# Kernel tuning notes

Measured on AMD Instinct MI355X. Metric: run time of the kernel, lower is better.

## Reference

```python
import jax, jax.numpy as jnp
import numpy as np

B, S, D, H, F, R = 4, 128, 512, 8, 2048, 8
DH = D // H
THRESH = 0.1  # hardcoded in the torch module


def _ln(x, g, b):
    m = x.mean(-1, keepdims=True)
    v = ((x - m) ** 2).mean(-1, keepdims=True)
    return (x - m) * jax.lax.rsqrt(v + 1e-5) * g + b


def setup_inputs() -> dict:
    key = jax.random.key(0)
    ks = jax.random.split(key, 12)
    w = lambda k, shape, std: jax.random.normal(k, shape, jnp.float32) * std
    s = 1.0 / np.sqrt(D)
    qk_std = 2.0 / np.sqrt(D)  # peaky attention so adjacency threshold fires
    return {
        "x": jax.random.normal(ks[0], (B, S, D), jnp.float32),
        "ln1_g": jnp.ones(D, jnp.float32), "ln1_b": jnp.zeros(D, jnp.float32),
        "wq": w(ks[1], (D, D), qk_std), "bq": jnp.zeros(D, jnp.float32),
        "wk": w(ks[2], (D, D), qk_std), "bk": jnp.zeros(D, jnp.float32),
        "wv": w(ks[3], (D, D), s), "bv": jnp.zeros(D, jnp.float32),
        "wo": w(ks[4], (D, D), s), "bo": jnp.zeros(D, jnp.float32),
        "w1": w(ks[5], (D, F), s), "b1": jnp.zeros(F, jnp.float32),
        "w2": w(ks[6], (F, D), 1.0 / np.sqrt(F)), "b2": jnp.zeros(D, jnp.float32),
        "rc_w1": w(ks[7], (2 * D, D), 1.0 / np.sqrt(2 * D)), "rc_b1": jnp.zeros(D, jnp.float32),
        "rc_w2": w(ks[8], (D, R), s), "rc_b2": jnp.zeros(R, jnp.float32),
        "kg_w": w(ks[9], (R, D, D), s),
        "s2n_w": w(ks[10], (D, D), s), "s2n_b": jnp.zeros(D, jnp.float32),
        "ln2_g": jnp.ones(D, jnp.float32), "ln2_b": jnp.zeros(D, jnp.float32),
    }


def reference(x, ln1_g, ln1_b, wq, bq, wk, bk, wv, bv, wo, bo,
              w1, b1, w2, b2, rc_w1, rc_b1, rc_w2, rc_b2,
              kg_w, s2n_w, s2n_b, ln2_g, ln2_b):
    # pre-norm attention
    xn = _ln(x, ln1_g, ln1_b)
    q = (xn @ wq + bq).reshape(B, S, H, DH)
    k = (xn @ wk + bk).reshape(B, S, H, DH)
    v = (xn @ wv + bv).reshape(B, S, H, DH)
    scores = jnp.einsum('bihd,bjhd->bhij', q, k) / np.sqrt(DH)
    attn = jax.nn.softmax(scores, axis=-1)                  # [B,H,S,S]
    ctx = jnp.einsum('bhij,bjhd->bihd', attn, v).reshape(B, S, D)
    attn_out = ctx @ wo + bo
    # FFN -> neural_understanding (no residual, as in source)
    nu = jax.nn.relu(attn_out @ w1 + b1) @ w2 + b2          # [B,S,D]
    # dynamic edge extraction, expressed as a dense mask (jit-safe)
    am = attn.mean(axis=1)                                  # [B,S,S]
    adj = (am > THRESH) & (~jnp.eye(S, dtype=bool))         # u != v
    # relation classifier on every (u,v) pair; mask selects real edges
    a_part = nu @ rc_w1[:D]                                 # concept1 half
    b_part = nu @ rc_w1[D:]                                 # concept2 half
    h = jax.nn.relu(a_part[:, :, None, :] + b_part[:, None, :, :] + rc_b1)  # [B,S,S,D]
    logits = h @ rc_w2 + rc_b2                              # [B,S,S,R]
    pred = jnp.argmax(logits, axis=-1)
    valid = adj & (pred != 0)                               # relation 0 == NONE
    oh = jax.nn.one_hot(pred, R, dtype=nu.dtype) * valid[..., None].astype(nu.dtype)
    # RGCN-style knowledge graph conv: message u -> v with per-relation weight
    transformed = jnp.einsum('bud,rde->bure', nu, kg_w)     # [B,S,R,D]
    agg = jnp.einsum('buvr,bure->bve', oh, transformed)     # [B,S,D]
    reasoned = nu + agg
    neural_result = reasoned @ s2n_w + s2n_b
    out = _ln(x + neural_result, ln2_g, ln2_b)
    return out
```

## Files before the change

kernel.cpp:

```cpp
#include <hip/hip_runtime.h>
#include <hip/hip_bf16.h>

#define B_ 4
#define S_ 128
#define D_ 512
#define H_ 8
#define DH_ 64
#define F_ 2048
#define R_ 8
#define BS_ (B_ * S_)
#define BSD_ (BS_ * D_)
#define E_ 262144

typedef __attribute__((ext_vector_type(8))) short short8;
typedef __attribute__((ext_vector_type(4))) float f32x4;
typedef __attribute__((ext_vector_type(4))) unsigned short ushort4v;

__device__ __forceinline__ void split2(float a, unsigned short& h, unsigned short& l) {
    unsigned u = __float_as_uint(a);
    unsigned hr = (u + 0x7FFFu + ((u >> 16) & 1u)) >> 16;
    h = (unsigned short)hr;
    float lo = a - __uint_as_float(hr << 16);
    unsigned u2 = __float_as_uint(lo);
    l = (unsigned short)((u2 + 0x7FFFu + ((u2 >> 16) & 1u)) >> 16);
}

struct TDesc { const float* s; unsigned short* h; unsigned short* l; int K; int N; int off; };
struct TPack { TDesc d[10]; };

__global__ void prep_kernel(TPack p, int nt, const float* __restrict__ x,
                            const float* __restrict__ g, const float* __restrict__ be,
                            unsigned short* __restrict__ xh, unsigned short* __restrict__ xl) {
    __shared__ float tr[32][33];
    __shared__ float red[256];
    int bid = blockIdx.x;
    if (bid < nt) {
        int wi = 0;
#pragma unroll
        for (int i = 1; i < 10; ++i) if (bid >= p.d[i].off) wi = i;
        const TDesc dd = p.d[wi];
        int t = bid - dd.off;
        int ntk = dd.K / 32;
        int tk = t % ntk, tn = t / ntk;
        int k0 = tk * 32, n0 = tn * 32;
        int col = threadIdx.x & 31, rg = threadIdx.x >> 5;
#pragma unroll
        for (int i = 0; i < 4; ++i) {
            int row = rg * 4 + i;
            tr[row][col] = dd.s[(size_t)(k0 + row) * dd.N + n0 + col];
        }
        __syncthreads();
#pragma unroll
        for (int i = 0; i < 4; ++i) {
            int n = n0 + rg * 4 + i;
            int k = k0 + col;
            unsigned short h, l;
            split2(tr[col][rg * 4 + i], h, l);
            dd.h[(size_t)n * dd.K + k] = h;
            dd.l[(size_t)n * dd.K + k] = l;
        }
    } else {
        int row = bid - nt;
        int t = threadIdx.x;
        const float* xr = x + (size_t)row * D_;
        float v0 = xr[t], v1 = xr[t + 256];
        red[t] = v0 + v1;
        __syncthreads();
        for (int off = 128; off > 0; off >>= 1) { if (t < off) red[t] += red[t + off]; __syncthreads(); }
        float mean = red[0] * (1.0f / D_);
        __syncthreads();
        float d0 = v0 - mean, d1 = v1 - mean;
        red[t] = d0 * d0 + d1 * d1;
        __syncthreads();
        for (int off = 128; off > 0; off >>= 1) { if (t < off) red[t] += red[t + off]; __syncthreads(); }
        float rs = rsqrtf(red[0] * (1.0f / D_) + 1e-5f);
        float o0 = d0 * rs * g[t] + be[t];
        float o1 = d1 * rs * g[t + 256] + be[t + 256];
        unsigned short h, l;
        split2(o0, h, l); xh[(size_t)row * D_ + t] = h;       xl[(size_t)row * D_ + t] = l;
        split2(o1, h, l); xh[(size_t)row * D_ + t + 256] = h; xl[(size_t)row * D_ + t + 256] = l;
    }
}

struct GemmLds {
    unsigned short A[2][2][64][32];
    unsigned short B[2][2][64][32];
};

__device__ __forceinline__ void gload16(const unsigned short* g, unsigned short* l) {
    __builtin_amdgcn_global_load_lds(
        (const __attribute__((address_space(1))) void*)g,
        (__attribute__((address_space(3))) void*)l, 16, 0, 0);
}

__device__ __forceinline__ void mgemm_core(const unsigned short* __restrict__ Ath,
                                           const unsigned short* __restrict__ Atl,
                                           const unsigned short* __restrict__ Bth,
                                           const unsigned short* __restrict__ Btl,
                                           int K, int rowBase, int colBase,
                                           int kStart, int nsteps,
                                           f32x4 acc[2][2], GemmLds* L) {
    int tid = threadIdx.x;
    int w = tid >> 6, lane = tid & 63;
    int lm = lane & 15, quad = lane >> 4;
    int wm = (w & 1) * 32, wn = (w >> 1) * 32;
    int rS = tid >> 2, kcS = (tid & 3) * 8;
    int wb = w * 512;
    size_t aoff = (size_t)(rowBase + rS) * K + kStart + kcS;
    size_t boff = (size_t)(colBase + rS) * K + kStart + kcS;
    gload16(&Ath[aoff], &L->A[0][0][0][0] + wb);
    gload16(&Atl[aoff], &L->A[0][1][0][0] + wb);
    gload16(&Bth[boff], &L->B[0][0][0][0] + wb);
    gload16(&Btl[boff], &L->B[0][1][0][0] + wb);
    __syncthreads();
    for (int s = 0; s < nsteps; ++s) {
        int p = s & 1;
        if (s + 1 < nsteps) {
            int pn = p ^ 1;
            size_t ao = aoff + (size_t)(s + 1) * 32;
            size_t bo = boff + (size_t)(s + 1) * 32;
            gload16(&Ath[ao], &L->A[pn][0][0][0] + wb);
            gload16(&Atl[ao], &L->A[pn][1][0][0] + wb);
            gload16(&Bth[bo], &L->B[pn][0][0][0] + wb);
            gload16(&Btl[bo], &L->B[pn][1][0][0] + wb);
        }
        short8 ah[2], al[2], bh[2], bl[2];
#pragma unroll
        for (int t = 0; t < 2; ++t) {
            ah[t] = *(const short8*)&L->A[p][0][wm + t * 16 + lm][quad * 8];
            al[t] = *(const short8*)&L->A[p][1][wm + t * 16 + lm][quad * 8];
            bh[t] = *(const short8*)&L->B[p][0][wn + t * 16 + lm][quad * 8];
            bl[t] = *(const short8*)&L->B[p][1][wn + t * 16 + lm][quad * 8];
        }
#pragma unroll
        for (int tm = 0; tm < 2; ++tm)
#pragma unroll
            for (int tn = 0; tn < 2; ++tn) {
                acc[tm][tn] = __builtin_amdgcn_mfma_f32_16x16x32_bf16(ah[tm], bh[tn], acc[tm][tn], 0, 0, 0);
                acc[tm][tn] = __builtin_amdgcn_mfma_f32_16x16x32_bf16(ah[tm], bl[tn], acc[tm][tn], 0, 0, 0);
                acc[tm][tn] = __builtin_amdgcn_mfma_f32_16x16x32_bf16(al[tm], bh[tn], acc[tm][tn], 0, 0, 0);
            }
        __syncthreads();
    }
}

__global__ __launch_bounds__(256) void mgemm_kernel(const unsigned short* __restrict__ Ath,
                                                    const unsigned short* __restrict__ Atl,
                                                    const unsigned short* __restrict__ Bth,
                                                    const unsigned short* __restrict__ Btl,
                                                    const float* __restrict__ bias,
                                                    float* __restrict__ Cf,
                                                    unsigned short* __restrict__ Ch,
                                                    unsigned short* __restrict__ Cl,
                                                    int N, int K, int relu) {
    __shared__ GemmLds L;
    int tid = threadIdx.x;
    int w = tid >> 6, lane = tid & 63;
    int lm = lane & 15, quad = lane >> 4;
    int wm = (w & 1) * 32, wn = (w >> 1) * 32;
    int rowBase = blockIdx.y * 64, colBase = blockIdx.x * 64;
    f32x4 acc[2][2] = {};
    mgemm_core(Ath, Atl, Bth, Btl, K, rowBase, colBase, 0, K / 32, acc, &L);
#pragma unroll
    for (int tm = 0; tm < 2; ++tm)
#pragma unroll
        for (int tn = 0; tn < 2; ++tn) {
            int col = colBase + wn + tn * 16 + lm;
            float bi = bias ? bias[col] : 0.f;
#pragma unroll
            for (int r = 0; r < 4; ++r) {
                int row = rowBase + wm + tm * 16 + quad * 4 + r;
                float v = acc[tm][tn][r] + bi;
                if (relu) v = fmaxf(v, 0.f);
                size_t o = (size_t)row * N + col;
                if (Cf) Cf[o] = v;
                if (Ch) {
                    unsigned short sh, sl;
                    split2(v, sh, sl);
                    Ch[o] = sh; Cl[o] = sl;
                }
            }
        }
}

__global__ __launch_bounds__(256) void mgemm_zw_kernel(const unsigned short* __restrict__ Ath,
                                                       const unsigned short* __restrict__ Atl,
                                                       const unsigned short* __restrict__ Bth,
                                                       const unsigned short* __restrict__ Btl,
                                                       const float* __restrict__ b0,
                                                       const float* __restrict__ b1,
                                                       const float* __restrict__ b2,
                                                       float* __restrict__ Cbase,
                                                       int M, int N, int K) {
    __shared__ GemmLds L;
    int z = blockIdx.z;
    const unsigned short* bth = Bth + (size_t)z * K * N;
    const unsigned short* btl = Btl + (size_t)z * K * N;
    const float* bias = (z == 0) ? b0 : (z == 1) ? b1 : b2;
    float* C = Cbase + (size_t)z * M * N;
    int tid = threadIdx.x;
    int w = tid >> 6, lane = tid & 63;
    int lm = lane & 15, quad = lane >> 4;
    int wm = (w & 1) * 32, wn = (w >> 1) * 32;
    int rowBase = blockIdx.y * 64, colBase = blockIdx.x * 64;
    f32x4 acc[2][2] = {};
    mgemm_core(Ath, Atl, bth, btl, K, rowBase, colBase, 0, K / 32, acc, &L);
#pragma unroll
    for (int tm = 0; tm < 2; ++tm)
#pragma unroll
        for (int tn = 0; tn < 2; ++tn) {
            int col = colBase + wn + tn * 16 + lm;
            float bi = bias ? bias[col] : 0.f;
#pragma unroll
            for (int r = 0; r < 4; ++r) {
                int row = rowBase + wm + tm * 16 + quad * 4 + r;
                C[(size_t)row * N + col] = acc[tm][tn][r] + bi;
            }
        }
}

__global__ __launch_bounds__(256) void mgemm_part_kernel(const unsigned short* __restrict__ Ath,
                                                         const unsigned short* __restrict__ Atl,
                                                         const unsigned short* __restrict__ Bth,
                                                         const unsigned short* __restrict__ Btl,
                                                         float* __restrict__ Cbase,
                                                         int M, int N, int K) {
    __shared__ GemmLds L;
    int ks = gridDim.z, z = blockIdx.z;
    int kLen = K / ks, kStart = z * kLen;
    float* C = Cbase + (size_t)z * M * N;
    int tid = threadIdx.x;
    int w = tid >> 6, lane = tid & 63;
    int lm = lane & 15, quad = lane >> 4;
    int wm = (w & 1) * 32, wn = (w >> 1) * 32;
    int rowBase = blockIdx.y * 64, colBase = blockIdx.x * 64;
    f32x4 acc[2][2] = {};
    mgemm_core(Ath, Atl, Bth, Btl, K, rowBase, colBase, kStart, kLen / 32, acc, &L);
#pragma unroll
    for (int tm = 0; tm < 2; ++tm)
#pragma unroll
        for (int tn = 0; tn < 2; ++tn) {
            int col = colBase + wn + tn * 16 + lm;
#pragma unroll
            for (int r = 0; r < 4; ++r) {
                int row = rowBase + wm + tm * 16 + quad * 4 + r;
                C[(size_t)row * N + col] = acc[tm][tn][r];
            }
        }
}

__global__ void reduce4_kernel(const float* __restrict__ part, const float* __restrict__ b2,
                               float* __restrict__ nu,
                               unsigned short* __restrict__ nh, unsigned short* __restrict__ nl) {
    int base = blockIdx.x * 1024 + threadIdx.x * 4;
    f32x4 s = *(const f32x4*)&b2[base & (D_ - 1)];
#pragma unroll
    for (int z = 0; z < 4; ++z) s += *(const f32x4*)&part[(size_t)z * BSD_ + base];
    *(f32x4*)&nu[base] = s;
    ushort4v hv, lv;
#pragma unroll
    for (int i = 0; i < 4; ++i) { unsigned short h, l; split2(s[i], h, l); hv[i] = h; lv[i] = l; }
    *(ushort4v*)&nh[base] = hv;
    *(ushort4v*)&nl[base] = lv;
}

__global__ void reduce8_kernel(const float* __restrict__ part, const float* __restrict__ nu,
                               unsigned short* __restrict__ rh, unsigned short* __restrict__ rl) {
    int base = blockIdx.x * 1024 + threadIdx.x * 4;
    f32x4 s = *(const f32x4*)&nu[base];
#pragma unroll
    for (int z = 0; z < 8; ++z) s += *(const f32x4*)&part[(size_t)z * BSD_ + base];
    ushort4v hv, lv;
#pragma unroll
    for (int i = 0; i < 4; ++i) { unsigned short h, l; split2(s[i], h, l); hv[i] = h; lv[i] = l; }
    *(ushort4v*)&rh[base] = hv;
    *(ushort4v*)&rl[base] = lv;
}

__global__ __launch_bounds__(512) void attn_fused_kernel(const float* __restrict__ q,
                                                         const float* __restrict__ k,
                                                         const float* __restrict__ v,
                                                         unsigned short* __restrict__ ch,
                                                         unsigned short* __restrict__ cl,
                                                         int* __restrict__ ecount,
                                                         int* __restrict__ elist) {
    __shared__ float qsm[H_][DH_];
    __shared__ float psm[H_][S_];
    int h = threadIdx.x >> 6, lane = threadIdx.x & 63;
    int blk = blockIdx.x;
    int i = blk & (S_ - 1);
    int b = blk >> 7;
    const float* qrow = q + (size_t)(b * S_ + i) * D_ + h * DH_;
    qsm[h][lane] = qrow[lane];
    __syncthreads();
    float s0 = 0.f, s1 = 0.f;
    const float* k0p = k + (size_t)(b * S_ + lane) * D_ + h * DH_;
    const float* k1p = k0p + (size_t)64 * D_;
#pragma unroll 8
    for (int d = 0; d < DH_; ++d) {
        float qd = qsm[h][d];
        s0 += qd * k0p[d];
        s1 += qd * k1p[d];
    }
    s0 *= 0.125f; s1 *= 0.125f;
    float m = fmaxf(s0, s1);
#pragma unroll
    for (int off = 32; off > 0; off >>= 1) m = fmaxf(m, __shfl_xor(m, off));
    float e0 = __expf(s0 - m), e1 = __expf(s1 - m);
    float sum = e0 + e1;
#pragma unroll
    for (int off = 32; off > 0; off >>= 1) sum += __shfl_xor(sum, off);
    float inv = 1.f / sum;
    psm[h][lane] = e0 * inv;
    psm[h][lane + 64] = e1 * inv;
    __syncthreads();
    if (threadIdx.x < S_) {
        int j = threadIdx.x;
        float s = 0.f;
#pragma unroll
        for (int hh = 0; hh < H_; ++hh) s += psm[hh][j];
        s *= (1.0f / H_);
        if (s > 0.1f && i != j) {
            int p = atomicAdd(ecount, 1);
            elist[p] = blk * S_ + j;
        }
    }
    const float* vbase = v + (size_t)b * S_ * D_ + h * DH_ + lane;
    float acc = 0.f;
    for (int j = 0; j < S_; ++j) acc += psm[h][j] * vbase[(size_t)j * D_];
    unsigned short sh, sl;
    split2(acc, sh, sl);
    size_t o = (size_t)(b * S_ + i) * D_ + h * DH_ + lane;
    ch[o] = sh; cl[o] = sl;
}

__global__ __launch_bounds__(256) void edge_kernel(const float* __restrict__ a_part,
                                                   const float* __restrict__ b_part,
                                                   const float* __restrict__ rc_b1,
                                                   const float* __restrict__ rc_w2,
                                                   const float* __restrict__ rc_b2,
                                                   const int* __restrict__ elist,
                                                   const int* __restrict__ ecount,
                                                   int* __restrict__ rel) {
    int w = threadIdx.x >> 6, lane = threadIdx.x & 63;
    int n = *ecount;
    for (int e = blockIdx.x * 4 + w; e < n; e += gridDim.x * 4) {
        int idx = elist[e];
        int vv = idx & (S_ - 1);
        int bu = idx >> 7;
        int u = bu & (S_ - 1);
        int b = bu >> 7;
        const float* ap = a_part + (size_t)(b * S_ + u) * D_;
        const float* bp = b_part + (size_t)(b * S_ + vv) * D_;
        float lp[R_];
#pragma unroll
        for (int r = 0; r < R_; ++r) lp[r] = 0.f;
#pragma unroll
        for (int jj = 0; jj < D_ / 64; ++jj) {
            int d = lane + jj * 64;
            float hv = fmaxf(ap[d] + bp[d] + rc_b1[d], 0.f);
#pragma unroll
            for (int r = 0; r < R_; ++r) lp[r] += hv * rc_w2[d * R_ + r];
        }
#pragma unroll
        for (int r = 0; r < R_; ++r) {
#pragma unroll
            for (int off = 32; off > 0; off >>= 1) lp[r] += __shfl_down(lp[r], off);
        }
        if (lane == 0) {
            float best = lp[0] + rc_b2[0];
            int bi = 0;
#pragma unroll
            for (int r = 1; r < R_; ++r) {
                float L = lp[r] + rc_b2[r];
                if (L > best) { best = L; bi = r; }
            }
            rel[idx] = bi;
        }
    }
}

__global__ __launch_bounds__(128) void mbuild_kernel(const float* __restrict__ nu,
                                                     const int* __restrict__ rel,
                                                     unsigned short* __restrict__ Mh,
                                                     unsigned short* __restrict__ Ml) {
    __shared__ float acc[R_ * D_];
    __shared__ int rl[S_];
    int blk = blockIdx.x;
    int vv = blk & (S_ - 1);
    int b = blk >> 7;
    int t = threadIdx.x;
    for (int i = t; i < R_ * D_; i += 128) acc[i] = 0.f;
    rl[t] = rel[((size_t)b * S_ + t) * S_ + vv];
    __syncthreads();
    for (int u = 0; u < S_; ++u) {
        int r = rl[u];
        if (r > 0) {
            const float* nurow = nu + (size_t)(b * S_ + u) * D_;
            float* arow = acc + r * D_;
#pragma unroll
            for (int jj = 0; jj < D_ / 128; ++jj) arow[t + jj * 128] += nurow[t + jj * 128];
        }
    }
    __syncthreads();
    unsigned short* Hrow = Mh + (size_t)blk * (R_ * D_);
    unsigned short* Lrow = Ml + (size_t)blk * (R_ * D_);
    for (int i = t; i < R_ * D_; i += 128) {
        unsigned short sh, sl;
        split2(acc[i], sh, sl);
        Hrow[i] = sh; Lrow[i] = sl;
    }
}

__global__ void ln2_kernel(const float* __restrict__ x, const float* __restrict__ y,
                           const float* __restrict__ g, const float* __restrict__ be,
                           float* __restrict__ out) {
    int row = blockIdx.x;
    int t = threadIdx.x;
    __shared__ float red[256];
    float v0 = x[row * D_ + t]       + y[row * D_ + t];
    float v1 = x[row * D_ + t + 256] + y[row * D_ + t + 256];
    red[t] = v0 + v1;
    __syncthreads();
    for (int off = 128; off > 0; off >>= 1) {
        if (t < off) red[t] += red[t + off];
        __syncthreads();
    }
    float mean = red[0] * (1.0f / D_);
    __syncthreads();
    float d0 = v0 - mean, d1 = v1 - mean;
    red[t] = d0 * d0 + d1 * d1;
    __syncthreads();
    for (int off = 128; off > 0; off >>= 1) {
        if (t < off) red[t] += red[t + off];
        __syncthreads();
    }
    float rs = rsqrtf(red[0] * (1.0f / D_) + 1e-5f);
    out[row * D_ + t]       = d0 * rs * g[t]       + be[t];
    out[row * D_ + t + 256] = d1 * rs * g[t + 256] + be[t + 256];
}

extern "C" void kernel_launch(void* const* d_in, const int* in_sizes, int n_in,
                              void* d_out, int out_size, void* d_ws, size_t ws_size,
                              hipStream_t stream) {
    const float* x     = (const float*)d_in[0];
    const float* ln1_g = (const float*)d_in[1];
    const float* ln1_b = (const float*)d_in[2];
    const float* wq    = (const float*)d_in[3];
    const float* bq    = (const float*)d_in[4];
    const float* wk    = (const float*)d_in[5];
    const float* bk    = (const float*)d_in[6];
    const float* wv    = (const float*)d_in[7];
    const float* bv    = (const float*)d_in[8];
    const float* wo    = (const float*)d_in[9];
    const float* bo    = (const float*)d_in[10];
    const float* w1    = (const float*)d_in[11];
    const float* b1    = (const float*)d_in[12];
    const float* w2    = (const float*)d_in[13];
    const float* b2    = (const float*)d_in[14];
    const float* rc_w1 = (const float*)d_in[15];
    const float* rc_b1 = (const float*)d_in[16];
    const float* rc_w2 = (const float*)d_in[17];
    const float* rc_b2 = (const float*)d_in[18];
    const float* kg_w  = (const float*)d_in[19];
    const float* s2n_w = (const float*)d_in[20];
    const float* s2n_b = (const float*)d_in[21];
    const float* ln2_g = (const float*)d_in[22];
    const float* ln2_b = (const float*)d_in[23];
    float* out = (float*)d_out;

    const int BS  = BS_;
    const int BSD = BSD_;

    unsigned short* wt = (unsigned short*)d_ws;
    unsigned short* qkv_h = wt;
    unsigned short* qkv_l = wt + 3 * E_;
    unsigned short* wo_h  = wt + 6 * E_;
    unsigned short* wo_l  = wt + 7 * E_;
    unsigned short* w1_h  = wt + 8 * E_;
    unsigned short* w1_l  = wt + 12 * E_;
    unsigned short* w2_h  = wt + 16 * E_;
    unsigned short* w2_l  = wt + 20 * E_;
    unsigned short* rc_h  = wt + 24 * E_;
    unsigned short* rc_l  = wt + 26 * E_;
    unsigned short* kg_h  = wt + 28 * E_;
    unsigned short* kg_l  = wt + 36 * E_;
    unsigned short* s2_h  = wt + 44 * E_;
    unsigned short* s2_l  = wt + 45 * E_;

    unsigned short* xn_h  = wt + 46 * E_;
    unsigned short* xn_l  = xn_h + BSD;
    unsigned short* ctx_h = xn_l + BSD;
    unsigned short* ctx_l = ctx_h + BSD;
    unsigned short* ao_h  = ctx_l + BSD;
    unsigned short* ao_l  = ao_h + BSD;
    unsigned short* hid_h = ao_l + BSD;
    unsigned short* hid_l = hid_h + (size_t)BS * F_;
    unsigned short* nu_h  = hid_l + (size_t)BS * F_;
    unsigned short* nu_l  = nu_h + BSD;
    unsigned short* mb_h  = nu_l + BSD;
    unsigned short* mb_l  = mb_h + (size_t)BS * R_ * D_;
    unsigned short* rs_h  = mb_l + (size_t)BS * R_ * D_;
    unsigned short* rs_l  = rs_h + BSD;

    float* fbase  = (float*)(rs_l + BSD);
    float* q      = fbase;
    float* v_     = q + 2 * BSD;
    float* apart  = q + 3 * BSD;
    float* nu     = apart + 2 * BSD;
    float* y      = nu + BSD;
    float* part4  = y + BSD;
    float* part8  = part4 + 4 * BSD;

    int* rel    = (int*)(part8 + 8 * BSD);
    int* ecount = rel + B_ * S_ * S_;
    int* elist  = ecount + 64;

    hipMemsetAsync(rel, 0, (size_t)(B_ * S_ * S_ + 64) * 4, stream);
    TPack tp;
    int off = 0;
    auto setd = [&](int i, const float* s, unsigned short* h, unsigned short* l, int K, int N) {
        tp.d[i] = TDesc{s, h, l, K, N, off};
        off += (K / 32) * (N / 32);
    };
    setd(0, wq, qkv_h,          qkv_l,          D_, D_);
    setd(1, wk, qkv_h + E_,     qkv_l + E_,     D_, D_);
    setd(2, wv, qkv_h + 2 * E_, qkv_l + 2 * E_, D_, D_);
    setd(3, wo, wo_h, wo_l, D_, D_);
    setd(4, w1, w1_h, w1_l, D_, F_);
    setd(5, w2, w2_h, w2_l, F_, D_);
    setd(6, rc_w1,            rc_h,      rc_l,      D_, D_);
    setd(7, rc_w1 + D_ * D_,  rc_h + E_, rc_l + E_, D_, D_);
    setd(8, kg_w, kg_h, kg_l, R_ * D_, D_);
    setd(9, s2n_w, s2_h, s2_l, D_, D_);
    hipLaunchKernelGGL(prep_kernel, dim3(off + BS), dim3(256), 0, stream, tp, off,
                       x, ln1_g, ln1_b, xn_h, xn_l);

    hipLaunchKernelGGL(mgemm_zw_kernel, dim3(D_ / 64, BS / 64, 3), dim3(256), 0, stream,
                       xn_h, xn_l, qkv_h, qkv_l, bq, bk, bv, q, BS, D_, D_);
    hipLaunchKernelGGL(attn_fused_kernel, dim3(BS), dim3(512), 0, stream,
                       q, q + BSD, v_, ctx_h, ctx_l, ecount, elist);
    hipLaunchKernelGGL(mgemm_kernel, dim3(D_ / 64, BS / 64), dim3(256), 0, stream,
                       ctx_h, ctx_l, wo_h, wo_l, bo, (float*)nullptr, ao_h, ao_l, D_, D_, 0);
    hipLaunchKernelGGL(mgemm_kernel, dim3(F_ / 64, BS / 64), dim3(256), 0, stream,
                       ao_h, ao_l, w1_h, w1_l, b1, (float*)nullptr, hid_h, hid_l, F_, D_, 1);
    hipLaunchKernelGGL(mgemm_part_kernel, dim3(D_ / 64, BS / 64, 4), dim3(256), 0, stream,
                       hid_h, hid_l, w2_h, w2_l, part4, BS, D_, F_);
    hipLaunchKernelGGL(reduce4_kernel, dim3(BSD / 1024), dim3(256), 0, stream,
                       part4, b2, nu, nu_h, nu_l);
    hipLaunchKernelGGL(mgemm_zw_kernel, dim3(D_ / 64, BS / 64, 2), dim3(256), 0, stream,
                       nu_h, nu_l, rc_h, rc_l, (const float*)nullptr, (const float*)nullptr,
                       (const float*)nullptr, apart, BS, D_, D_);
    hipLaunchKernelGGL(edge_kernel, dim3(256), dim3(256), 0, stream,
                       apart, apart + BSD, rc_b1, rc_w2, rc_b2, elist, ecount, rel);
    hipLaunchKernelGGL(mbuild_kernel, dim3(BS), dim3(128), 0, stream, nu, rel, mb_h, mb_l);
    hipLaunchKernelGGL(mgemm_part_kernel, dim3(D_ / 64, BS / 64, 8), dim3(256), 0, stream,
                       mb_h, mb_l, kg_h, kg_l, part8, BS, D_, R_ * D_);
    hipLaunchKernelGGL(reduce8_kernel, dim3(BSD / 1024), dim3(256), 0, stream,
                       part8, nu, rs_h, rs_l);
    hipLaunchKernelGGL(mgemm_kernel, dim3(D_ / 64, BS / 64), dim3(256), 0, stream,
                       rs_h, rs_l, s2_h, s2_l, s2n_b, y, (unsigned short*)nullptr,
                       (unsigned short*)nullptr, D_, D_, 0);
    hipLaunchKernelGGL(ln2_kernel, dim3(BS), dim3(256), 0, stream, x, y, ln2_g, ln2_b, out);
}
```

Measured before the change: 251.3 us.

## Unify GEMMs into split-K kernel with last-block atomic reduction

Replaces the separate GEMM, partial-GEMM and reduce kernels with one split-K kernel. Blocks write fp32 partials, and the last block for each tile, found through an atomic counter, sums them and applies bias, residual, relu and the bf16 split. This removes the two standalone reduce launches and raises block counts for the small 512x512 GEMMs to fill more CUs. The cost is extra partial-buffer traffic, thread fences, and a serialized reduction done by the last-arriving block.

```diff
diff --git a/kernel.cpp b/kernel.cpp
--- a/kernel.cpp
+++ b/kernel.cpp
@@ -144,23 +144,83 @@
     }
 }
 
-__global__ __launch_bounds__(256) void mgemm_kernel(const unsigned short* __restrict__ Ath,
-                                                    const unsigned short* __restrict__ Atl,
-                                                    const unsigned short* __restrict__ Bth,
-                                                    const unsigned short* __restrict__ Btl,
-                                                    const float* __restrict__ bias,
-                                                    float* __restrict__ Cf,
-                                                    unsigned short* __restrict__ Ch,
-                                                    unsigned short* __restrict__ Cl,
-                                                    int N, int K, int relu) {
+__global__ __launch_bounds__(256) void mg_kernel(const unsigned short* __restrict__ Ath,
+                                                 const unsigned short* __restrict__ Atl,
+                                                 const unsigned short* __restrict__ Bth,
+                                                 const unsigned short* __restrict__ Btl,
+                                                 const float* __restrict__ b0,
+                                                 const float* __restrict__ b1,
+                                                 const float* __restrict__ b2,
+                                                 const float* __restrict__ res,
+                                                 float* __restrict__ Cf,
+                                                 unsigned short* __restrict__ Ch,
+                                                 unsigned short* __restrict__ Cl,
+                                                 float* __restrict__ part,
+                                                 int* __restrict__ flags,
+                                                 int nz, int N, int K, int relu) {
     __shared__ GemmLds L;
+    __shared__ int smLast;
+    int ks = gridDim.z / nz;
+    int slab = blockIdx.z / ks, split = blockIdx.z - slab * ks;
+    int M = gridDim.y * 64;
+    const unsigned short* bth = Bth + (size_t)slab * K * N;
+    const unsigned short* btl = Btl + (size_t)slab * K * N;
+    const float* bias = (slab == 0) ? b0 : (slab == 1) ? b1 : b2;
+    size_t slabOff = (size_t)slab * M * N;
+    int kLen = K / ks;
     int tid = threadIdx.x;
     int w = tid >> 6, lane = tid & 63;
     int lm = lane & 15, quad = lane >> 4;
     int wm = (w & 1) * 32, wn = (w >> 1) * 32;
     int rowBase = blockIdx.y * 64, colBase = blockIdx.x * 64;
     f32x4 acc[2][2] = {};
-    mgemm_core(Ath, Atl, Bth, Btl, K, rowBase, colBase, 0, K / 32, acc, &L);
+    mgemm_core(Ath, Atl, bth, btl, K, rowBase, colBase, split * kLen, kLen / 32, acc, &L);
+
+    if (ks == 1) {
+#pragma unroll
+        for (int tm = 0; tm < 2; ++tm)
+#pragma unroll
+            for (int tn = 0; tn < 2; ++tn) {
+                int col = colBase + wn + tn * 16 + lm;
+                float bi = bias ? bias[col] : 0.f;
+#pragma unroll
+                for (int r = 0; r < 4; ++r) {
+                    int row = rowBase + wm + tm * 16 + quad * 4 + r;
+                    size_t o = (size_t)row * N + col;
+                    float v = acc[tm][tn][r] + bi;
+                    if (res) v += res[slabOff + o];
+                    if (relu) v = fmaxf(v, 0.f);
+                    if (Cf) Cf[slabOff + o] = v;
+                    if (Ch) {
+                        unsigned short sh, sl;
+                        split2(v, sh, sl);
+                        Ch[slabOff + o] = sh; Cl[slabOff + o] = sl;
+                    }
+                }
+            }
+        return;
+    }
+    float* myPart = part + (size_t)(slab * ks + split) * M * N;
+#pragma unroll
+    for (int tm = 0; tm < 2; ++tm)
+#pragma unroll
+        for (int tn = 0; tn < 2; ++tn) {
+            int col = colBase + wn + tn * 16 + lm;
+#pragma unroll
+            for (int r = 0; r < 4; ++r) {
+                int row = rowBase + wm + tm * 16 + quad * 4 + r;
+                myPart[(size_t)row * N + col] = acc[tm][tn][r];
+            }
+        }
+    __threadfence();
+    __syncthreads();
+    if (tid == 0) {
+        int fi = slab * gridDim.x * gridDim.y + blockIdx.y * gridDim.x + blockIdx.x;
+        smLast = (atomicAdd(&flags[fi], 1) == ks - 1);
+    }
+    __syncthreads();
+    if (!smLast) return;
+    __threadfence();
 #pragma unroll
     for (int tm = 0; tm < 2; ++tm)
 #pragma unroll
@@ -170,111 +230,19 @@
 #pragma unroll
             for (int r = 0; r < 4; ++r) {
                 int row = rowBase + wm + tm * 16 + quad * 4 + r;
-                float v = acc[tm][tn][r] + bi;
-                if (relu) v = fmaxf(v, 0.f);
                 size_t o = (size_t)row * N + col;
-                if (Cf) Cf[o] = v;
+                float s = res ? res[slabOff + o] : bi;
+                for (int z = 0; z < ks; ++z)
+                    s += part[(size_t)(slab * ks + z) * M * N + o];
+                if (relu) s = fmaxf(s, 0.f);
+                if (Cf) Cf[slabOff + o] = s;
                 if (Ch) {
                     unsigned short sh, sl;
-                    split2(v, sh, sl);
-                    Ch[o] = sh; Cl[o] = sl;
+                    split2(s, sh, sl);
+                    Ch[slabOff + o] = sh; Cl[slabOff + o] = sl;
                 }
             }
         }
-}
-
-__global__ __launch_bounds__(256) void mgemm_zw_kernel(const unsigned short* __restrict__ Ath,
-                                                       const unsigned short* __restrict__ Atl,
-                                                       const unsigned short* __restrict__ Bth,
-                                                       const unsigned short* __restrict__ Btl,
-                                                       const float* __restrict__ b0,
-                                                       const float* __restrict__ b1,
-                                                       const float* __restrict__ b2,
-                                                       float* __restrict__ Cbase,
-                                                       int M, int N, int K) {
-    __shared__ GemmLds L;
-    int z = blockIdx.z;
-    const unsigned short* bth = Bth + (size_t)z * K * N;
-    const unsigned short* btl = Btl + (size_t)z * K * N;
-    const float* bias = (z == 0) ? b0 : (z == 1) ? b1 : b2;
-    float* C = Cbase + (size_t)z * M * N;
-    int tid = threadIdx.x;
-    int w = tid >> 6, lane = tid & 63;
-    int lm = lane & 15, quad = lane >> 4;
-    int wm = (w & 1) * 32, wn = (w >> 1) * 32;
-    int rowBase = blockIdx.y * 64, colBase = blockIdx.x * 64;
-    f32x4 acc[2][2] = {};
-    mgemm_core(Ath, Atl, bth, btl, K, rowBase, colBase, 0, K / 32, acc, &L);
-#pragma unroll
-    for (int tm = 0; tm < 2; ++tm)
-#pragma unroll
-        for (int tn = 0; tn < 2; ++tn) {
-            int col = colBase + wn + tn * 16 + lm;
-            float bi = bias ? bias[col] : 0.f;
-#pragma unroll
-            for (int r = 0; r < 4; ++r) {
-                int row = rowBase + wm + tm * 16 + quad * 4 + r;
-                C[(size_t)row * N + col] = acc[tm][tn][r] + bi;
-            }
-        }
-}
-
-__global__ __launch_bounds__(256) void mgemm_part_kernel(const unsigned short* __restrict__ Ath,
-                                                         const unsigned short* __restrict__ Atl,
-                                                         const unsigned short* __restrict__ Bth,
-                                                         const unsigned short* __restrict__ Btl,
-                                                         float* __restrict__ Cbase,
-                                                         int M, int N, int K) {
-    __shared__ GemmLds L;
-    int ks = gridDim.z, z = blockIdx.z;
-    int kLen = K / ks, kStart = z * kLen;
-    float* C = Cbase + (size_t)z * M * N;
-    int tid = threadIdx.x;
-    int w = tid >> 6, lane = tid & 63;
-    int lm = lane & 15, quad = lane >> 4;
-    int wm = (w & 1) * 32, wn = (w >> 1) * 32;
-    int rowBase = blockIdx.y * 64, colBase = blockIdx.x * 64;
-    f32x4 acc[2][2] = {};
-    mgemm_core(Ath, Atl, Bth, Btl, K, rowBase, colBase, kStart, kLen / 32, acc, &L);
-#pragma unroll
-    for (int tm = 0; tm < 2; ++tm)
-#pragma unroll
-        for (int tn = 0; tn < 2; ++tn) {
-            int col = colBase + wn + tn * 16 + lm;
-#pragma unroll
-            for (int r = 0; r < 4; ++r) {
-                int row = rowBase + wm + tm * 16 + quad * 4 + r;
-                C[(size_t)row * N + col] = acc[tm][tn][r];
-            }
-        }
-}
-
-__global__ void reduce4_kernel(const float* __restrict__ part, const float* __restrict__ b2,
-                               float* __restrict__ nu,
-                               unsigned short* __restrict__ nh, unsigned short* __restrict__ nl) {
-    int base = blockIdx.x * 1024 + threadIdx.x * 4;
-    f32x4 s = *(const f32x4*)&b2[base & (D_ - 1)];
-#pragma unroll
-    for (int z = 0; z < 4; ++z) s += *(const f32x4*)&part[(size_t)z * BSD_ + base];
-    *(f32x4*)&nu[base] = s;
-    ushort4v hv, lv;
-#pragma unroll
-    for (int i = 0; i < 4; ++i) { unsigned short h, l; split2(s[i], h, l); hv[i] = h; lv[i] = l; }
-    *(ushort4v*)&nh[base] = hv;
-    *(ushort4v*)&nl[base] = lv;
-}
-
-__global__ void reduce8_kernel(const float* __restrict__ part, const float* __restrict__ nu,
-                               unsigned short* __restrict__ rh, unsigned short* __restrict__ rl) {
-    int base = blockIdx.x * 1024 + threadIdx.x * 4;
-    f32x4 s = *(const f32x4*)&nu[base];
-#pragma unroll
-    for (int z = 0; z < 8; ++z) s += *(const f32x4*)&part[(size_t)z * BSD_ + base];
-    ushort4v hv, lv;
-#pragma unroll
-    for (int i = 0; i < 4; ++i) { unsigned short h, l; split2(s[i], h, l); hv[i] = h; lv[i] = l; }
-    *(ushort4v*)&rh[base] = hv;
-    *(ushort4v*)&rl[base] = lv;
 }
 
 __global__ __launch_bounds__(512) void attn_fused_kernel(const float* __restrict__ q,
@@ -471,6 +439,8 @@
 
     const int BS  = BS_;
     const int BSD = BSD_;
+    const float* fnull = nullptr;
+    unsigned short* unull = nullptr;
 
     unsigned short* wt = (unsigned short*)d_ws;
     unsigned short* qkv_h = wt;
@@ -509,14 +479,22 @@
     float* apart  = q + 3 * BSD;
     float* nu     = apart + 2 * BSD;
     float* y      = nu + BSD;
-    float* part4  = y + BSD;
-    float* part8  = part4 + 4 * BSD;
-
-    int* rel    = (int*)(part8 + 8 * BSD);
+    float* part   = y + BSD;
+
+    int* rel    = (int*)(part + 8 * BSD);
     int* ecount = rel + B_ * S_ * S_;
-    int* elist  = ecount + 64;
-
-    hipMemsetAsync(rel, 0, (size_t)(B_ * S_ * S_ + 64) * 4, stream);
+    int* flags  = ecount + 64;
+    int* elist  = flags + 1024;
+
+    int* fQKV  = flags;
+    int* fWO   = flags + 192;
+    int* fFFN1 = flags + 256;
+    int* fFFN2 = flags + 512;
+    int* fRC   = flags + 576;
+    int* fKG   = flags + 704;
+    int* fS2N  = flags + 768;
+
+    hipMemsetAsync(rel, 0, (size_t)(B_ * S_ * S_ + 64 + 1024) * 4, stream);
     TPack tp;
     int off = 0;
     auto setd = [&](int i, const float* s, unsigned short* h, unsigned short* l, int K, int N) {
@@ -536,30 +514,31 @@
     hipLaunchKernelGGL(prep_kernel, dim3(off + BS), dim3(256), 0, stream, tp, off,
                        x, ln1_g, ln1_b, xn_h, xn_l);
 
-    hipLaunchKernelGGL(mgemm_zw_kernel, dim3(D_ / 64, BS / 64, 3), dim3(256), 0, stream,
-                       xn_h, xn_l, qkv_h, qkv_l, bq, bk, bv, q, BS, D_, D_);
+    hipLaunchKernelGGL(mg_kernel, dim3(D_ / 64, BS / 64, 6), dim3(256), 0, stream,
+                       xn_h, xn_l, qkv_h, qkv_l, bq, bk, bv, fnull,
+                       q, unull, unull, part, fQKV, 3, D_, D_, 0);
     hipLaunchKernelGGL(attn_fused_kernel, dim3(BS), dim3(512), 0, stream,
                        q, q + BSD, v_, ctx_h, ctx_l, ecount, elist);
-    hipLaunchKernelGGL(mgemm_kernel, dim3(D_ / 64, BS / 64), dim3(256), 0, stream,
-                       ctx_h, ctx_l, wo_h, wo_l, bo, (float*)nullptr, ao_h, ao_l, D_, D_, 0);
-    hipLaunchKernelGGL(mgemm_kernel, dim3(F_ / 64, BS / 64), dim3(256), 0, stream,
-                       ao_h, ao_l, w1_h, w1_l, b1, (float*)nullptr, hid_h, hid_l, F_, D_, 1);
-    hipLaunchKernelGGL(mgemm_part_kernel, dim3(D_ / 64, BS / 64, 4), dim3(256), 0, stream,
-                       hid_h, hid_l, w2_h, w2_l, part4, BS, D_, F_);
-    hipLaunchKernelGGL(reduce4_kernel, dim3(BSD / 1024), dim3(256), 0, stream,
-                       part4, b2, nu, nu_h, nu_l);
-    hipLaunchKernelGGL(mgemm_zw_kernel, dim3(D_ / 64, BS / 64, 2), dim3(256), 0, stream,
-                       nu_h, nu_l, rc_h, rc_l, (const float*)nullptr, (const float*)nullptr,
-                       (const float*)nullptr, apart, BS, D_, D_);
+    hipLaunchKernelGGL(mg_kernel, dim3(D_ / 64, BS / 64, 4), dim3(256), 0, stream,
+                       ctx_h, ctx_l, wo_h, wo_l, bo, fnull, fnull, fnull,
+                       (float*)nullptr, ao_h, ao_l, part, fWO, 1, D_, D_, 0);
+    hipLaunchKernelGGL(mg_kernel, dim3(F_ / 64, BS / 64, 2), dim3(256), 0, stream,
+                       ao_h, ao_l, w1_h, w1_l, b1, fnull, fnull, fnull,
+                       (float*)nullptr, hid_h, hid_l, part, fFFN1, 1, F_, D_, 1);
+    hipLaunchKernelGGL(mg_kernel, dim3(D_ / 64, BS / 64, 4), dim3(256), 0, stream,
+                       hid_h, hid_l, w2_h, w2_l, b2, fnull, fnull, fnull,
+                       nu, nu_h, nu_l, part, fFFN2, 1, D_, F_, 0);
+    hipLaunchKernelGGL(mg_kernel, dim3(D_ / 64, BS / 64, 4), dim3(256), 0, stream,
+                       nu_h, nu_l, rc_h, rc_l, fnull, fnull, fnull, fnull,
+                       apart, unull, unull, part, fRC, 2, D_, D_, 0);
     hipLaunchKernelGGL(edge_kernel, dim3(256), dim3(256), 0, stream,
                        apart, apart + BSD, rc_b1, rc_w2, rc_b2, elist, ecount, rel);
     hipLaunchKernelGGL(mbuild_kernel, dim3(BS), dim3(128), 0, stream, nu, rel, mb_h, mb_l);
-    hipLaunchKernelGGL(mgemm_part_kernel, dim3(D_ / 64, BS / 64, 8), dim3(256), 0, stream,
-                       mb_h, mb_l, kg_h, kg_l, part8, BS, D_, R_ * D_);
-    hipLaunchKernelGGL(reduce8_kernel, dim3(BSD / 1024), dim3(256), 0, stream,
-                       part8, nu, rs_h, rs_l);
-    hipLaunchKernelGGL(mgemm_kernel, dim3(D_ / 64, BS / 64), dim3(256), 0, stream,
-                       rs_h, rs_l, s2_h, s2_l, s2n_b, y, (unsigned short*)nullptr,
-                       (unsigned short*)nullptr, D_, D_, 0);
+    hipLaunchKernelGGL(mg_kernel, dim3(D_ / 64, BS / 64, 8), dim3(256), 0, stream,
+                       mb_h, mb_l, kg_h, kg_l, fnull, fnull, fnull, nu,
+                       (float*)nullptr, rs_h, rs_l, part, fKG, 1, D_, R_ * D_, 0);
+    hipLaunchKernelGGL(mg_kernel, dim3(D_ / 64, BS / 64, 4), dim3(256), 0, stream,
+                       rs_h, rs_l, s2_h, s2_l, s2n_b, fnull, fnull, fnull,
+                       y, unull, unull, part, fS2N, 1, D_, D_, 0);
     hipLaunchKernelGGL(ln2_kernel, dim3(BS), dim3(256), 0, stream, x, y, ln2_g, ln2_b, out);
 }
```

Result: slower. 606.2 us (+141.2%).
